# Kernel tuning notes

Measured on AMD Instinct MI355X. Metric: run time of the kernel, lower is better.

## Reference

```python
import jax, jax.numpy as jnp
import numpy as np

TWO_PI = 2.0 * np.pi
E_PHI = jnp.array([0.0, 0.0, 1.0, 0.0], dtype=jnp.float32)  # one-hot for phi slot


def calc_bbox(x):
    pt, rap, phi, m = jnp.split(x, 4, -1)
    pt = jnp.exp(jnp.minimum(pt, 10.0))
    m = jnp.exp(jnp.minimum(m, 10.0))
    rap = jax.nn.sigmoid(rap) * TWO_PI
    phi = jax.nn.sigmoid(phi) * TWO_PI
    return jnp.concatenate([pt, rap, phi, m], -1)


def momentum_l1(pred_raw, tgt):
    # pred_raw: [N,1,4] raw, tgt: [1,M,4] already in bbox form
    p = calc_bbox(pred_raw)
    te = jnp.where(p[..., 2] - tgt[..., 2] > np.pi, TWO_PI, 0.0)[..., None] * E_PHI
    pe = jnp.where(tgt[..., 2] - p[..., 2] > np.pi, TWO_PI, 0.0)[..., None] * E_PHI
    err = (p + jax.lax.stop_gradient(pe)) / (tgt + jax.lax.stop_gradient(te) + 0.001)
    return jnp.mean(jnp.abs(err - 1.0), -1)  # [N,M]


def eiou(pred_raw, tgt):
    w1, x1, y1, h1 = jnp.split(calc_bbox(pred_raw), 4, -1)
    w2, x2, y2, h2 = jnp.split(tgt, 4, -1)
    y1e = jnp.where(y2 - y1 > np.pi, TWO_PI, 0.0)
    y2e = jnp.where(y1 - y2 > np.pi, TWO_PI, 0.0)
    y1 = y1 + y1e
    y2 = y2 + y2e
    w = jnp.minimum(x1 + w1 / 2, x2 + w2 / 2) - jnp.maximum(x1 - w1 / 2, x2 - w2 / 2)
    h = jnp.minimum(y1 + h1 / 2, y2 + h2 / 2) - jnp.maximum(y1 - h1 / 2, y2 - h2 / 2)
    iou = jnp.where((w > 0) & (h > 0), w * h / (w1 * h1 + w2 * h2 - w * h + 0.001), 0.0)
    cw2 = jnp.square(jnp.maximum(x1 + w1 / 2, x2 + w2 / 2) - jnp.minimum(x1 - w1 / 2, x2 - w2 / 2))
    ch2 = jnp.square(jnp.maximum(y1 + h1 / 2, y2 + h2 / 2) - jnp.minimum(y1 - h1 / 2, y2 - h2 / 2))
    rho_w = jnp.square(w1 - w2) / (cw2 + 0.001)
    rho_h = jnp.square(h1 - h2) / (ch2 + 0.001)
    rho_d = (jnp.square(x1 - x2) + jnp.square(y1 - y2)) / (cw2 + ch2 + 0.001)
    return (1.0 - iou + rho_d + rho_w + rho_h).squeeze(-1)  # [N,M]


def _cost_matrix(pred_prob, pred_mask, pred_momentum, target_class, target_mask, target_momentum):
    B, N = pred_mask.shape[:2]
    H, W = target_mask.shape[-2:]
    # torch F.interpolate(mode='bilinear', align_corners=False) == jax bilinear resize
    pm = jax.image.resize(pred_mask, (B, N, H, W), method='bilinear')

    def per_batch(prob, mask, mom, tcls, tmask, tmom):
        # prob: [C,N], tcls: [M] -> cost_class: [N,M] (with_logits=False: already probs)
        cost_class = -prob[tcls].T
        p = mask[:, None]   # [N,1,H,W]
        t = tmask[None]     # [1,M,H,W]
        # dice semimetric over (H,W)
        neg = jnp.sum(jnp.abs(p - t), (-2, -1))                                   # [N,M]
        pos = jnp.sum(jnp.abs(mask), (-2, -1))[:, None] + jnp.sum(jnp.abs(tmask), (-2, -1))[None]
        cost_dice = 1.0 - (pos - neg) / (pos + 0.001)
        # focal (alpha=0.25, gamma=2), mean over (H,W)
        pc = jnp.clip(p, 0.001, 0.999)
        pt_ = pc * t + (1 - pc) * (1 - t)
        ce = -(t * jnp.log(pc) + (1 - t) * jnp.log(1 - pc))
        at = 0.25 * t + 0.75 * (1 - t)
        cost_focal = jnp.mean(at * ce * jnp.square(1 - pt_), (-2, -1))            # [N,M]
        pmom = mom[:, None]    # [N,1,4] raw
        tmom_b = tmom[None]    # [1,M,4] bbox-space
        cost_l1 = momentum_l1(pmom, tmom_b)
        cost_eiou = eiou(pmom, tmom_b)
        cost = (0.25 * cost_focal + 0.75 * cost_dice + 1.0 * cost_class
                + 0.8 * cost_l1 + 0.2 * cost_eiou)
        return jnp.where(tcls[None, :] > 0, cost, 100000.0)

    return jax.vmap(per_batch)(pred_prob, pm, pred_momentum, target_class, target_mask, target_momentum)


def setup_inputs() -> dict:
    key = jax.random.key(0)
    ks = jax.random.split(key, 6)
    B, C, N, M = 2, 10, 100, 50
    Hp, Wp, H, W = 24, 24, 96, 96
    pred_prob = jax.random.uniform(ks[0], (B, C, N), dtype=jnp.float32)
    pred_mask = jax.random.uniform(ks[1], (B, N, Hp, Wp), dtype=jnp.float32)
    pred_momentum = jax.random.normal(ks[2], (B, N, 4), dtype=jnp.float32)
    target_class = jax.random.randint(ks[3], (B, M), 0, C)
    target_mask = jnp.round(jax.random.uniform(ks[4], (B, M, H, W), dtype=jnp.float32))
    target_momentum = calc_bbox(jax.random.normal(ks[5], (B, M, 4), dtype=jnp.float32))
    return {"pred_prob": pred_prob, "pred_mask": pred_mask, "pred_momentum": pred_momentum,
            "target_class": target_class, "target_mask": target_mask, "target_momentum": target_momentum}


def reference(pred_prob, pred_mask, pred_momentum, target_class, target_mask, target_momentum):
    return _cost_matrix(pred_prob, pred_mask, pred_momentum, target_class, target_mask, target_momentum)
```

## Files before the change

kernel.cpp:

```cpp
#include <hip/hip_runtime.h>
#include <math.h>

#define BB 2
#define CC 10
#define NN 100
#define MM 50
#define HP 24
#define WP 24
#define HH 96
#define WW 96
#define HW (HH*WW)
#define KCHUNKS 32
#define CHUNK (HW/KCHUNKS)
#define KC 32
#define NSTEPS (CHUNK/KC)
#define PAD 36

static __device__ __forceinline__ float dot4(float4 a, float4 b) {
    return a.x*b.x + a.y*b.y + a.z*b.z + a.w*b.w;
}

__global__ __launch_bounds__(256) void k_pre(
    const float* __restrict__ pm,
    const float* __restrict__ tm,
    float* __restrict__ Q, float* __restrict__ D,
    float* __restrict__ sumP, float* __restrict__ sumF0,
    float* __restrict__ tsum)
{
    const int tid = threadIdx.x;
    __shared__ float tile[HP*WP];
    __shared__ float red[8];

    if (blockIdx.x >= BB*NN) {
        const int bm = blockIdx.x - BB*NN;
        const float4* t4 = (const float4*)(tm + (size_t)bm * HW);
        float s = 0.f;
#pragma unroll
        for (int i = 0; i < 9; ++i) {
            float4 v = t4[i*256 + tid];
            s += v.x + v.y + v.z + v.w;
        }
#pragma unroll
        for (int o = 32; o > 0; o >>= 1) s += __shfl_down(s, o);
        const int wid = tid >> 6, lane = tid & 63;
        if (lane == 0) red[wid] = s;
        __syncthreads();
        if (tid == 0) tsum[bm] = red[0] + red[1] + red[2] + red[3];
        return;
    }

    const int bn = blockIdx.x;
    const float* in = pm + (size_t)bn * (HP*WP);
    for (int i = tid; i < HP*WP; i += 256) tile[i] = in[i];
    __syncthreads();

    float* q = Q + (size_t)bn * HW;
    float* d = D + (size_t)bn * HW;

    float sp = 0.f, sf = 0.f;
#pragma unroll 4
    for (int s = 0; s < HW/256; ++s) {
        const int idx = s*256 + tid;
        const int i = idx / WW;
        const int j = idx - i*WW;
        float y = (i + 0.5f)*0.25f - 0.5f;
        float x = (j + 0.5f)*0.25f - 0.5f;
        y = fminf(fmaxf(y, 0.f), 23.f);
        x = fminf(fmaxf(x, 0.f), 23.f);
        const int y0 = (int)y;
        const int x0 = (int)x;
        const float fy = y - (float)y0;
        const float fx = x - (float)x0;
        const int y1 = (y0 < HP-1) ? y0+1 : HP-1;
        const int x1 = (x0 < WP-1) ? x0+1 : WP-1;
        const float v00 = tile[y0*WP + x0], v01 = tile[y0*WP + x1];
        const float v10 = tile[y1*WP + x0], v11 = tile[y1*WP + x1];
        const float p = (1.f-fy)*((1.f-fx)*v00 + fx*v01)
                      +       fy*((1.f-fx)*v10 + fx*v11);

        const float pc  = fminf(fmaxf(p, 0.001f), 0.999f);
        const float omc = 1.f - pc;
        const float f1 = 0.25f * (-logf(pc))  * omc*omc;
        const float f0 = 0.75f * (-logf(omc)) * pc*pc;

        q[idx] = 1.f - 2.f*p;
        d[idx] = f1 - f0;
        sp += p;
        sf += f0;
    }

#pragma unroll
    for (int o = 32; o > 0; o >>= 1) {
        sp += __shfl_down(sp, o);
        sf += __shfl_down(sf, o);
    }
    const int wid = tid >> 6, lane = tid & 63;
    if (lane == 0) { red[wid] = sp; red[4+wid] = sf; }
    __syncthreads();
    if (tid == 0) {
        sumP[bn]  = red[0] + red[1] + red[2] + red[3];
        sumF0[bn] = red[4] + red[5] + red[6] + red[7];
    }
}

__global__ __launch_bounds__(256) void k_dots(
    const float* __restrict__ Q, const float* __restrict__ D,
    const float* __restrict__ T,
    float* __restrict__ pNeg, float* __restrict__ pF)
{
    const int kc = blockIdx.x;
    const int nt = blockIdx.y >> 1;
    const int mt = blockIdx.y & 1;
    const int b  = blockIdx.z;
    const int tid = threadIdx.x;
    const int ni = tid >> 4;
    const int mi = tid & 15;

    __shared__ float tS[32][PAD];
    __shared__ float qS[32][PAD];
    __shared__ float dS[32][PAD];

    const int n0 = nt*32, m0 = mt*32;
    const int k0 = kc*CHUNK;

    const int lr = tid >> 3;
    const int lc = (tid & 7) * 4;

    float accN[2][2] = {{0.f,0.f},{0.f,0.f}};
    float accF[2][2] = {{0.f,0.f},{0.f,0.f}};

    for (int s = 0; s < NSTEPS; ++s) {
        const int kb = k0 + s*KC;
        {
            const int n = n0 + lr;
            float4 qa = {0,0,0,0}, da = {0,0,0,0};
            if (n < NN) {
                qa = *(const float4*)(Q + ((size_t)b*NN + n)*HW + kb + lc);
                da = *(const float4*)(D + ((size_t)b*NN + n)*HW + kb + lc);
            }
            *(float4*)&qS[lr][lc] = qa;
            *(float4*)&dS[lr][lc] = da;

            const int m = m0 + lr;
            float4 ta = {0,0,0,0};
            if (m < MM) {
                ta = *(const float4*)(T + ((size_t)b*MM + m)*HW + kb + lc);
            }
            *(float4*)&tS[lr][lc] = ta;
        }
        __syncthreads();
#pragma unroll
        for (int kk = 0; kk < KC; kk += 4) {
            const float4 t0 = *(const float4*)&tS[mi   ][kk];
            const float4 t1 = *(const float4*)&tS[mi+16][kk];
            const float4 q0 = *(const float4*)&qS[ni   ][kk];
            const float4 q1 = *(const float4*)&qS[ni+16][kk];
            const float4 d0 = *(const float4*)&dS[ni   ][kk];
            const float4 d1 = *(const float4*)&dS[ni+16][kk];
            accN[0][0] += dot4(q0, t0);  accN[0][1] += dot4(q0, t1);
            accN[1][0] += dot4(q1, t0);  accN[1][1] += dot4(q1, t1);
            accF[0][0] += dot4(d0, t0);  accF[0][1] += dot4(d0, t1);
            accF[1][0] += dot4(d1, t0);  accF[1][1] += dot4(d1, t1);
        }
        __syncthreads();
    }

#pragma unroll
    for (int a = 0; a < 2; ++a)
#pragma unroll
        for (int c = 0; c < 2; ++c) {
            const int n = n0 + ni + a*16;
            const int m = m0 + mi + c*16;
            if (n < NN && m < MM) {
                const size_t o = (((size_t)kc*BB + b)*NN + n)*MM + m;
                pNeg[o] = accN[a][c];
                pF[o]   = accF[a][c];
            }
        }
}

__global__ __launch_bounds__(256) void k_final(
    const float* __restrict__ pNeg, const float* __restrict__ pF,
    const float* __restrict__ sumP, const float* __restrict__ sumF0,
    const float* __restrict__ tsum,
    const float* __restrict__ prob,
    const float* __restrict__ pmom,
    const int*   __restrict__ tcls,
    const float* __restrict__ tmom,
    float* __restrict__ out)
{
    const int idx = blockIdx.x*256 + threadIdx.x;
    if (idx >= BB*NN*MM) return;
    const int m = idx % MM;
    const int n = (idx / MM) % NN;
    const int b = idx / (NN*MM);

    const float PI_F     = 3.14159265358979323846f;
    const float TWO_PI_F = 6.28318530717958647692f;

    float nd = 0.f, fd = 0.f;
#pragma unroll
    for (int kc = 0; kc < KCHUNKS; ++kc) {
        const size_t o = (((size_t)kc*BB + b)*NN + n)*MM + m;
        nd += pNeg[o];
        fd += pF[o];
    }
    const float sp  = sumP[b*NN + n];
    const float sf0 = sumF0[b*NN + n];
    const float ts  = tsum[b*MM + m];

    const float neg = sp + nd;
    const float pos = sp + ts;
    const float cost_dice  = 1.f - (pos - neg) / (pos + 0.001f);
    const float cost_focal = (sf0 + fd) * (1.f / (float)HW);

    const int tc = tcls[b*MM + m];
    const float cost_class = -prob[((size_t)b*CC + tc)*NN + n];

    const float* pr = pmom + ((size_t)b*NN + n)*4;
    const float p0 = expf(fminf(pr[0], 10.f));
    const float p1 = TWO_PI_F / (1.f + expf(-pr[1]));
    const float p2 = TWO_PI_F / (1.f + expf(-pr[2]));
    const float p3 = expf(fminf(pr[3], 10.f));

    const float* tg = tmom + ((size_t)b*MM + m)*4;
    const float t0 = tg[0], t1 = tg[1], t2 = tg[2], t3 = tg[3];

    const float te2 = (p2 - t2 > PI_F) ? TWO_PI_F : 0.f;
    const float pe2 = (t2 - p2 > PI_F) ? TWO_PI_F : 0.f;
    const float e0 = p0 / (t0 + 0.001f);
    const float e1 = p1 / (t1 + 0.001f);
    const float e2 = (p2 + pe2) / (t2 + te2 + 0.001f);
    const float e3 = p3 / (t3 + 0.001f);
    const float cost_l1 = 0.25f * (fabsf(e0 - 1.f) + fabsf(e1 - 1.f)
                                 + fabsf(e2 - 1.f) + fabsf(e3 - 1.f));

    const float w1 = p0, x1 = p1, y1o = p2, h1 = p3;
    const float w2 = t0, x2 = t1, y2o = t2, h2 = t3;
    const float y1 = y1o + ((y2o - y1o > PI_F) ? TWO_PI_F : 0.f);
    const float y2 = y2o + ((y1o - y2o > PI_F) ? TWO_PI_F : 0.f);

    const float xr1 = x1 + w1*0.5f, xl1 = x1 - w1*0.5f;
    const float xr2 = x2 + w2*0.5f, xl2 = x2 - w2*0.5f;
    const float yr1 = y1 + h1*0.5f, yl1 = y1 - h1*0.5f;
    const float yr2 = y2 + h2*0.5f, yl2 = y2 - h2*0.5f;

    const float wi = fminf(xr1, xr2) - fmaxf(xl1, xl2);
    const float hi = fminf(yr1, yr2) - fmaxf(yl1, yl2);
    const float iou = (wi > 0.f && hi > 0.f)
        ? wi*hi / (w1*h1 + w2*h2 - wi*hi + 0.001f) : 0.f;

    const float cw = fmaxf(xr1, xr2) - fminf(xl1, xl2);
    const float ch = fmaxf(yr1, yr2) - fminf(yl1, yl2);
    const float cw2 = cw*cw, ch2 = ch*ch;
    const float rho_w = (w1 - w2)*(w1 - w2) / (cw2 + 0.001f);
    const float rho_h = (h1 - h2)*(h1 - h2) / (ch2 + 0.001f);
    const float rho_d = ((x1 - x2)*(x1 - x2) + (y1 - y2)*(y1 - y2))
                        / (cw2 + ch2 + 0.001f);
    const float cost_eiou = 1.f - iou + rho_d + rho_w + rho_h;

    const float cost = 0.25f*cost_focal + 0.75f*cost_dice + cost_class
                     + 0.8f*cost_l1 + 0.2f*cost_eiou;
    out[idx] = (tc > 0) ? cost : 100000.0f;
}

extern "C" void kernel_launch(void* const* d_in, const int* in_sizes, int n_in,
                              void* d_out, int out_size, void* d_ws, size_t ws_size,
                              hipStream_t stream) {
    const float* pred_prob  = (const float*)d_in[0];
    const float* pred_mask  = (const float*)d_in[1];
    const float* pred_mom   = (const float*)d_in[2];
    const int*   tgt_class  = (const int*)  d_in[3];
    const float* tgt_mask   = (const float*)d_in[4];
    const float* tgt_mom    = (const float*)d_in[5];
    float* out = (float*)d_out;

    float* ws    = (float*)d_ws;
    float* Q     = ws;
    float* D     = Q + (size_t)BB*NN*HW;
    float* sumP  = D + (size_t)BB*NN*HW;
    float* sumF0 = sumP + BB*NN;
    float* tsum  = sumF0 + BB*NN;
    float* pNeg  = tsum + BB*MM;
    float* pF    = pNeg + (size_t)KCHUNKS*BB*NN*MM;

    k_pre  <<<BB*NN + BB*MM, 256, 0, stream>>>(
        pred_mask, tgt_mask, Q, D, sumP, sumF0, tsum);
    k_dots <<<dim3(KCHUNKS, 8, BB), 256, 0, stream>>>(Q, D, tgt_mask, pNeg, pF);
    k_final<<<(BB*NN*MM + 255)/256, 256, 0, stream>>>(
        pNeg, pF, sumP, sumF0, tsum,
        pred_prob, pred_mom, tgt_class, tgt_mom, out);
}
```

Measured before the change: 99.85 us.

## Fuse bilinear upsample and focal terms into dot kernel, drop Q/D buffers

Stops materialising the upsampled Q and D arrays (two fields of 200x9216 floats) in global memory. Instead, each k_dots block loads the few low-res mask rows covering its K chunk into shared memory and recomputes the interpolation and focal logs on the fly. This removes roughly 15 MB of global write and read traffic. In exchange, transcendental work is recomputed once per m-tile (twice) and the loop adds a barrier and extra LDS reads.

```diff
diff --git a/kernel.cpp b/kernel.cpp
--- a/kernel.cpp
+++ b/kernel.cpp
@@ -15,6 +15,7 @@
 #define KC 32
 #define NSTEPS (CHUNK/KC)
 #define PAD 36
+#define PMPAD 76
 
 static __device__ __forceinline__ float dot4(float4 a, float4 b) {
     return a.x*b.x + a.y*b.y + a.z*b.z + a.w*b.w;
@@ -23,7 +24,6 @@
 __global__ __launch_bounds__(256) void k_pre(
     const float* __restrict__ pm,
     const float* __restrict__ tm,
-    float* __restrict__ Q, float* __restrict__ D,
     float* __restrict__ sumP, float* __restrict__ sumF0,
     float* __restrict__ tsum)
 {
@@ -53,9 +53,6 @@
     const float* in = pm + (size_t)bn * (HP*WP);
     for (int i = tid; i < HP*WP; i += 256) tile[i] = in[i];
     __syncthreads();
-
-    float* q = Q + (size_t)bn * HW;
-    float* d = D + (size_t)bn * HW;
 
     float sp = 0.f, sf = 0.f;
 #pragma unroll 4
@@ -80,13 +77,8 @@
 
         const float pc  = fminf(fmaxf(p, 0.001f), 0.999f);
         const float omc = 1.f - pc;
-        const float f1 = 0.25f * (-logf(pc))  * omc*omc;
-        const float f0 = 0.75f * (-logf(omc)) * pc*pc;
-
-        q[idx] = 1.f - 2.f*p;
-        d[idx] = f1 - f0;
         sp += p;
-        sf += f0;
+        sf += 0.75f * (-logf(omc)) * pc*pc;
     }
 
 #pragma unroll
@@ -104,7 +96,7 @@
 }
 
 __global__ __launch_bounds__(256) void k_dots(
-    const float* __restrict__ Q, const float* __restrict__ D,
+    const float* __restrict__ pm,
     const float* __restrict__ T,
     float* __restrict__ pNeg, float* __restrict__ pF)
 {
@@ -116,12 +108,36 @@
     const int ni = tid >> 4;
     const int mi = tid & 15;
 
+    __shared__ float pmS[32][PMPAD];
     __shared__ float tS[32][PAD];
     __shared__ float qS[32][PAD];
     __shared__ float dS[32][PAD];
 
     const int n0 = nt*32, m0 = mt*32;
     const int k0 = kc*CHUNK;
+    const int i0 = 3*kc;
+
+    const float ymin = fminf(fmaxf(((float)i0 + 0.5f)*0.25f - 0.5f, 0.f), 23.f);
+    const int r0 = (int)ymin;
+
+#pragma unroll
+    for (int it = 0; it < 3; ++it) {
+        const int q = it*256 + tid;
+        if (q < 32*3*6) {
+            const int n   = q / 18;
+            const int rem = q - n*18;
+            const int r   = rem / 6;
+            const int c4  = rem - r*6;
+            const int gn  = n0 + n;
+            float4 v = {0,0,0,0};
+            if (gn < NN) {
+                const int row = (r0 + r < HP-1) ? r0 + r : HP-1;
+                v = *(const float4*)(pm + ((size_t)b*NN + gn)*(HP*WP)
+                                        + row*WP + c4*4);
+            }
+            *(float4*)&pmS[n][r*WP + c4*4] = v;
+        }
+    }
 
     const int lr = tid >> 3;
     const int lc = (tid & 7) * 4;
@@ -131,22 +147,43 @@
 
     for (int s = 0; s < NSTEPS; ++s) {
         const int kb = k0 + s*KC;
+        __syncthreads();
         {
-            const int n = n0 + lr;
-            float4 qa = {0,0,0,0}, da = {0,0,0,0};
-            if (n < NN) {
-                qa = *(const float4*)(Q + ((size_t)b*NN + n)*HW + kb + lc);
-                da = *(const float4*)(D + ((size_t)b*NN + n)*HW + kb + lc);
-            }
-            *(float4*)&qS[lr][lc] = qa;
-            *(float4*)&dS[lr][lc] = da;
-
             const int m = m0 + lr;
             float4 ta = {0,0,0,0};
             if (m < MM) {
                 ta = *(const float4*)(T + ((size_t)b*MM + m)*HW + kb + lc);
             }
             *(float4*)&tS[lr][lc] = ta;
+
+#pragma unroll
+            for (int u = 0; u < 4; ++u) {
+                const int ke = s*KC + lc + u;
+                const int di = ke / WW;
+                const int j  = ke - di*WW;
+                const int i  = i0 + di;
+                float y = ((float)i + 0.5f)*0.25f - 0.5f;
+                float x = ((float)j + 0.5f)*0.25f - 0.5f;
+                y = fminf(fmaxf(y, 0.f), 23.f);
+                x = fminf(fmaxf(x, 0.f), 23.f);
+                const int y0 = (int)y;
+                const int x0 = (int)x;
+                const float fy = y - (float)y0;
+                const float fx = x - (float)x0;
+                const int yi0 = y0 - r0;
+                const int yi1 = ((y0 < HP-1) ? y0+1 : HP-1) - r0;
+                const int x1  = (x0 < WP-1) ? x0+1 : WP-1;
+                const float v00 = pmS[lr][yi0*WP + x0], v01 = pmS[lr][yi0*WP + x1];
+                const float v10 = pmS[lr][yi1*WP + x0], v11 = pmS[lr][yi1*WP + x1];
+                const float p = (1.f-fy)*((1.f-fx)*v00 + fx*v01)
+                              +       fy*((1.f-fx)*v10 + fx*v11);
+                const float pc  = fminf(fmaxf(p, 0.001f), 0.999f);
+                const float omc = 1.f - pc;
+                const float f1 = 0.25f * (-logf(pc))  * omc*omc;
+                const float f0 = 0.75f * (-logf(omc)) * pc*pc;
+                qS[lr][lc+u] = 1.f - 2.f*p;
+                dS[lr][lc+u] = f1 - f0;
+            }
         }
         __syncthreads();
 #pragma unroll
@@ -162,7 +199,6 @@
             accF[0][0] += dot4(d0, t0);  accF[0][1] += dot4(d0, t1);
             accF[1][0] += dot4(d1, t0);  accF[1][1] += dot4(d1, t1);
         }
-        __syncthreads();
     }
 
 #pragma unroll
@@ -276,17 +312,16 @@
     float* out = (float*)d_out;
 
     float* ws    = (float*)d_ws;
-    float* Q     = ws;
-    float* D     = Q + (size_t)BB*NN*HW;
-    float* sumP  = D + (size_t)BB*NN*HW;
+    float* sumP  = ws;
     float* sumF0 = sumP + BB*NN;
     float* tsum  = sumF0 + BB*NN;
     float* pNeg  = tsum + BB*MM;
     float* pF    = pNeg + (size_t)KCHUNKS*BB*NN*MM;
 
     k_pre  <<<BB*NN + BB*MM, 256, 0, stream>>>(
-        pred_mask, tgt_mask, Q, D, sumP, sumF0, tsum);
-    k_dots <<<dim3(KCHUNKS, 8, BB), 256, 0, stream>>>(Q, D, tgt_mask, pNeg, pF);
+        pred_mask, tgt_mask, sumP, sumF0, tsum);
+    k_dots <<<dim3(KCHUNKS, 8, BB), 256, 0, stream>>>(
+        pred_mask, tgt_mask, pNeg, pF);
     k_final<<<(BB*NN*MM + 255)/256, 256, 0, stream>>>(
         pNeg, pF, sumP, sumF0, tsum,
         pred_prob, pred_mom, tgt_class, tgt_mom, out);
```

Result: no change. 99.75 us (-0.1%).
